# Optimization experiments

Hardware: AMD Instinct MI355X
Metric: run time of the kernel (lower is better)

## Reference

```python
import jax, jax.numpy as jnp
import numpy as np

B, T, S = 4, 128, 8192
HID, NH, NKV, HD = 2560, 8, 4, 256
INTER = 10240
WINDOW = 1024
SOFTCAP = 50.0
SCALING = 256 ** -0.5  # query_pre_attn_scalar ** -0.5
EPS = 1e-6
NEG = -2.3819763e38  # large negative for masking (matches Gemma mask value)
ROPE_THETA = 10000.0


def _rmsnorm(x, w):
    xf = x.astype(jnp.float32)
    o = xf * jax.lax.rsqrt(jnp.mean(xf * xf, axis=-1, keepdims=True) + EPS)
    return (o * (1.0 + w.astype(jnp.float32))).astype(x.dtype)


def _rope(x, cos, sin):
    # split-half rotation, matching torch apply_rotary_emb (chunk->complex->mul)
    d2 = x.shape[-1] // 2
    x1, x2 = x[..., :d2], x[..., d2:]
    c = cos[None, :, None, :]  # [1,T,1,D/2]
    s = sin[None, :, None, :]
    return jnp.concatenate([x1 * c - x2 * s, x1 * s + x2 * c], axis=-1)


def setup_inputs() -> dict:
    key = jax.random.key(0)
    ks = jax.random.split(key, 14)
    hidden_states = jax.random.normal(ks[0], (B, T, HID), jnp.float32)
    kv_write_indices = jnp.arange(T, dtype=jnp.int32)
    k_cache = jnp.zeros((B, S, NKV, HD), jnp.float32)
    v_cache = jnp.zeros((B, S, NKV, HD), jnp.float32)
    # rotary tables for positions 0..T-1
    inv = 1.0 / (ROPE_THETA ** (np.arange(0, HD, 2)[: HD // 2].astype(np.float32) / HD))
    fr = np.outer(np.arange(T, dtype=np.float32), inv).astype(np.float32)
    freqs_cos = jnp.asarray(np.cos(fr))
    freqs_sin = jnp.asarray(np.sin(fr))
    # masks: query i sits at absolute position i; cache slots >= T are unwritten
    qpos = jnp.arange(T)[:, None]
    kpos = jnp.arange(S)[None, :]
    causal = kpos <= qpos
    local = causal & ((qpos - kpos) < WINDOW)
    mask = jnp.broadcast_to(jnp.where(causal, 0.0, NEG)[None, None], (B, 1, T, S)).astype(jnp.float32)
    local_mask = jnp.broadcast_to(jnp.where(local, 0.0, NEG)[None, None], (B, 1, T, S)).astype(jnp.float32)
    sc = 0.02
    w_qkv = sc * jax.random.normal(ks[1], ((NH + 2 * NKV) * HD, HID), jnp.float32)
    w_o = sc * jax.random.normal(ks[2], (HID, NH * HD), jnp.float32)
    q_norm_w = 0.1 * jax.random.normal(ks[3], (HD,), jnp.float32)
    k_norm_w = 0.1 * jax.random.normal(ks[4], (HD,), jnp.float32)
    in_ln_w = 0.1 * jax.random.normal(ks[5], (HID,), jnp.float32)
    post_attn_ln_w = 0.1 * jax.random.normal(ks[6], (HID,), jnp.float32)
    pre_ffw_ln_w = 0.1 * jax.random.normal(ks[7], (HID,), jnp.float32)
    post_ffw_ln_w = 0.1 * jax.random.normal(ks[8], (HID,), jnp.float32)
    w_gate = sc * jax.random.normal(ks[9], (INTER, HID), jnp.float32)
    w_up = sc * jax.random.normal(ks[10], (INTER, HID), jnp.float32)
    w_down = sc * jax.random.normal(ks[11], (HID, INTER), jnp.float32)
    return {
        "hidden_states": hidden_states, "freqs_cos": freqs_cos, "freqs_sin": freqs_sin,
        "kv_write_indices": kv_write_indices, "k_cache": k_cache, "v_cache": v_cache,
        "mask": mask, "local_mask": local_mask,
        "w_qkv": w_qkv, "w_o": w_o, "q_norm_w": q_norm_w, "k_norm_w": k_norm_w,
        "in_ln_w": in_ln_w, "post_attn_ln_w": post_attn_ln_w,
        "pre_ffw_ln_w": pre_ffw_ln_w, "post_ffw_ln_w": post_ffw_ln_w,
        "w_gate": w_gate, "w_up": w_up, "w_down": w_down,
    }


def reference(hidden_states, freqs_cos, freqs_sin, kv_write_indices, k_cache, v_cache,
              mask, local_mask, w_qkv, w_o, q_norm_w, k_norm_w, in_ln_w,
              post_attn_ln_w, pre_ffw_ln_w, post_ffw_ln_w, w_gate, w_up, w_down):
    b, t, _ = hidden_states.shape
    residual = hidden_states
    h = _rmsnorm(hidden_states, in_ln_w)
    qkv = h @ w_qkv.T
    q_sz, kv_sz = NH * HD, NKV * HD
    xq = qkv[..., :q_sz].reshape(b, t, NH, HD)
    xk = qkv[..., q_sz:q_sz + kv_sz].reshape(b, t, NKV, HD)
    xv = qkv[..., q_sz + kv_sz:].reshape(b, t, NKV, HD)
    xq = _rmsnorm(xq, q_norm_w)  # QK-norm
    xk = _rmsnorm(xk, k_norm_w)
    xq = _rope(xq, freqs_cos, freqs_sin)
    xk = _rope(xk, freqs_cos, freqs_sin)
    kc = k_cache.at[:, kv_write_indices].set(xk)  # index_copy_ on dim 1
    vc = v_cache.at[:, kv_write_indices].set(xv)
    g = NH // NKV
    q = (xq * SCALING).reshape(b, t, NKV, g, HD)
    # GQA without repeat_interleave: group dim g shares each kv head
    scores = jnp.einsum('btkgd,bskd->bkgts', q, kc)
    scores = SOFTCAP * jnp.tanh(scores / SOFTCAP)  # logit softcapping
    scores = scores + local_mask[:, :, None]  # LOCAL_SLIDING -> use local mask
    probs = jax.nn.softmax(scores.astype(jnp.float32), axis=-1).astype(q.dtype)
    attn = jnp.einsum('bkgts,bskd->btkgd', probs, vc).reshape(b, t, NH * HD)
    attn = attn @ w_o.T
    h = residual + _rmsnorm(attn, post_attn_ln_w)
    residual = h
    x = _rmsnorm(h, pre_ffw_ln_w)
    gate = jax.nn.gelu(x @ w_gate.T, approximate=True)
    mlp = (gate * (x @ w_up.T)) @ w_down.T
    return residual + _rmsnorm(mlp, post_ffw_ln_w)
```

## Files before the change

kernel.cpp:

```cpp
#include <hip/hip_runtime.h>
#include <hip/hip_bf16.h>

#define B_ 4
#define T_ 128
#define HID 2560
#define NH 8
#define NKV 4
#define HD 256
#define INTER 10240
#define MROWS 512
#define EPS 1e-6f

typedef float f32x4 __attribute__((ext_vector_type(4)));
typedef __bf16 bf16x8 __attribute__((ext_vector_type(8)));

__device__ __forceinline__ unsigned short f2bf(float f){
  unsigned int u = __builtin_bit_cast(unsigned int, f);
  u += 0x7fffu + ((u >> 16) & 1u);
  return (unsigned short)(u >> 16);
}
__device__ __forceinline__ float bf2f(unsigned short u){
  unsigned int x = ((unsigned int)u) << 16;
  return __builtin_bit_cast(float, x);
}
__device__ __forceinline__ unsigned int cvtpk(float lo, float hi){
  unsigned int r;
  asm("v_cvt_pk_bf16_f32 %0, %1, %2" : "=v"(r) : "v"(lo), "v"(hi));
  return r;
}

__device__ __forceinline__ float bsum256(float v, float* buf){
  #pragma unroll
  for (int o = 32; o; o >>= 1) v += __shfl_xor(v, o);
  __syncthreads();
  if ((threadIdx.x & 63) == 0) buf[threadIdx.x >> 6] = v;
  __syncthreads();
  return buf[0] + buf[1] + buf[2] + buf[3];
}


__global__ __launch_bounds__(256) void rms_in(
    const float* __restrict__ x, const float* __restrict__ w,
    unsigned short* __restrict__ out)
{
  __shared__ float buf[4];
  const int r = blockIdx.x, tid = threadIdx.x;
  const float* xp = x + (size_t)r * HID;
  float v[10]; float ss = 0.f;
  #pragma unroll
  for (int j = 0; j < 10; j++){ v[j] = xp[tid + j*256]; ss += v[j]*v[j]; }
  ss = bsum256(ss, buf);
  float s = rsqrtf(ss * (1.f/HID) + EPS);
  #pragma unroll
  for (int j = 0; j < 10; j++){
    int i = tid + j*256;
    out[((size_t)(i >> 5) * MROWS + r) * 32 + (i & 31)] = f2bf(v[j] * s * (1.f + w[i]));
  }
}

__global__ __launch_bounds__(256, 2) void gemm_big(
    const unsigned short* __restrict__ Ap,
    const float* __restrict__ B0,
    const float* __restrict__ B1,
    int n_hi,
    unsigned short* __restrict__ C,
    int N, int K, int klen)
{
  __shared__ char Bs[2][128*64];
  const int tid = threadIdx.x;
  const int bid = (blockIdx.x & 7) * ((int)gridDim.x >> 3) + (blockIdx.x >> 3);
  const int bm = (bid & 1) << 8;
  const int bn = (bid >> 1) << 7;
  const int kt0 = (blockIdx.y * klen) >> 5;
  const int nt = klen >> 5;

  const int srow = tid >> 1, shalf = tid & 1;
  const float* Bb = (bn < n_hi) ? B0 : B1;
  const int bnr = (bn < n_hi) ? bn : (bn - n_hi);
  const float* BpG = Bb + (size_t)(bnr + srow) * K + (kt0 << 5) + (shalf << 4);

  const int wave = tid >> 6, lane = tid & 63;
  const int wm = (wave & 1) << 7;
  const int wn = (wave >> 1) << 6;
  const int fr = lane & 15, kq = lane >> 4;
  const int bslot = ((kq ^ ((fr >> 1) & 3)) << 4);
  const int brsw = (srow >> 1) & 3;
  const int s0 = (((2*shalf)     ^ brsw) << 4);
  const int s1 = (((2*shalf + 1) ^ brsw) << 4);

  const unsigned short* ApL = Ap + ((size_t)kt0 * MROWS + bm + wm + fr) * 32 + kq * 8;

  f32x4 acc[8][4];
  #pragma unroll
  for (int i = 0; i < 8; i++)
    #pragma unroll
    for (int j = 0; j < 4; j++)
      #pragma unroll
      for (int e = 0; e < 4; e++) acc[i][j][e] = 0.f;

  uint4 aR[8], aS[8];
  float4 rb0, rb1, rb2, rb3, sb0, sb1, sb2, sb3;

#define ISSUE_A(dst, tt) { const unsigned short* ap = ApL + (size_t)(tt) * 16384; \
  dst[0] = *(const uint4*)(ap);        dst[1] = *(const uint4*)(ap + 512); \
  dst[2] = *(const uint4*)(ap + 1024); dst[3] = *(const uint4*)(ap + 1536); \
  dst[4] = *(const uint4*)(ap + 2048); dst[5] = *(const uint4*)(ap + 2560); \
  dst[6] = *(const uint4*)(ap + 3072); dst[7] = *(const uint4*)(ap + 3584); }
#define LOAD_B(p0,p1,p2,p3, tt) { const float* bp = BpG + ((tt) << 5); \
  p0 = *(const float4*)(bp);     p1 = *(const float4*)(bp + 4); \
  p2 = *(const float4*)(bp + 8); p3 = *(const float4*)(bp + 12); }
#define WRITE_B(cur, b0,b1,b2,b3) { uint4 w0, w1; \
  w0.x = cvtpk(b0.x,b0.y); w0.y = cvtpk(b0.z,b0.w); \
  w0.z = cvtpk(b1.x,b1.y); w0.w = cvtpk(b1.z,b1.w); \
  w1.x = cvtpk(b2.x,b2.y); w1.y = cvtpk(b2.z,b2.w); \
  w1.z = cvtpk(b3.x,b3.y); w1.w = cvtpk(b3.z,b3.w); \
  char* bbase = &Bs[cur][srow*64]; \
  *(uint4*)(bbase + s0) = w0; \
  *(uint4*)(bbase + s1) = w1; }
#define BAR() { asm volatile("s_waitcnt lgkmcnt(0)" ::: "memory"); \
  __builtin_amdgcn_s_barrier(); }
#define COMPUTE(cur, aset) { const char* bb = Bs[cur]; \
  bf16x8 bfv[4]; \
  _Pragma("unroll") for (int ni = 0; ni < 4; ni++) \
    bfv[ni] = *(const bf16x8*)(bb + ((wn + ni*16 + fr) << 6) + bslot); \
  __builtin_amdgcn_s_setprio(1); \
  _Pragma("unroll") for (int mi = 0; mi < 8; mi++){ \
    bf16x8 af = __builtin_bit_cast(bf16x8, aset[mi]); \
    _Pragma("unroll") for (int ni = 0; ni < 4; ni++) \
      acc[mi][ni] = __builtin_amdgcn_mfma_f32_16x16x32_bf16(af, bfv[ni], acc[mi][ni], 0, 0, 0); } \
  __builtin_amdgcn_s_setprio(0); }

  ISSUE_A(aR, 0);
  LOAD_B(rb0,rb1,rb2,rb3, 0);
  LOAD_B(sb0,sb1,sb2,sb3, 1);

  for (int t = 0; t < nt; t += 2) {
    ISSUE_A(aS, t + 1);
    WRITE_B(0, rb0,rb1,rb2,rb3);
    BAR();
    if (t + 2 < nt) LOAD_B(rb0,rb1,rb2,rb3, t + 2);
    COMPUTE(0, aR);
    if (t + 2 < nt) ISSUE_A(aR, t + 2);
    WRITE_B(1, sb0,sb1,sb2,sb3);
    BAR();
    if (t + 3 < nt) LOAD_B(sb0,sb1,sb2,sb3, t + 3);
    COMPUTE(1, aS);
  }
#undef ISSUE_A
#undef LOAD_B
#undef WRITE_B
#undef BAR
#undef COMPUTE

  unsigned short* Cp = C + (size_t)blockIdx.y * MROWS * N;
  #pragma unroll
  for (int mi = 0; mi < 8; mi++) {
    #pragma unroll
    for (int ni = 0; ni < 4; ni++) {
      int m = bm + wm + mi*16 + kq*4;
      int n = bn + wn + ni*16 + fr;
      #pragma unroll
      for (int i = 0; i < 4; i++)
        Cp[(size_t)(m + i) * N + n] = f2bf(acc[mi][ni][i]);
    }
  }
}

__global__ __launch_bounds__(64) void qkv_post(
    const unsigned short* __restrict__ qkvp,
    const float* __restrict__ fcos, const float* __restrict__ fsin,
    const float* __restrict__ qnw, const float* __restrict__ knw,
    float* __restrict__ qout, float* __restrict__ kT, float* __restrict__ vout)
{
  const int row = blockIdx.x;
  const int hh  = blockIdx.y;
  const int b = row >> 7, t = row & 127;
  const int l = threadIdx.x;
  const size_t MS = (size_t)MROWS * 4096;
  const unsigned short* src = qkvp + (size_t)row * 4096 + hh * 256;
  float x[4];
  #pragma unroll
  for (int j = 0; j < 4; j++){
    int d = l + j*64;
    float v = 0.f;
    #pragma unroll
    for (int s = 0; s < 8; s++) v += bf2f(src[d + s*MS]);
    x[j] = v;
  }
  if (hh >= 12) {
    float* vp = vout + ((size_t)(b*NKV + (hh-12)) * T_ + t) * HD;
    #pragma unroll
    for (int j = 0; j < 4; j++) vp[l + j*64] = x[j];
    return;
  }
  float ss = x[0]*x[0] + x[1]*x[1] + x[2]*x[2] + x[3]*x[3];
  #pragma unroll
  for (int o = 32; o; o >>= 1) ss += __shfl_xor(ss, o);
  float r = rsqrtf(ss * (1.f/HD) + EPS);
  const float* nw = (hh < 8) ? qnw : knw;
  #pragma unroll
  for (int j = 0; j < 4; j++){ int d = l + j*64; x[j] = x[j] * r * (1.f + nw[d]); }
  float c0 = fcos[t*128 + l],      s0 = fsin[t*128 + l];
  float c1 = fcos[t*128 + l + 64], s1 = fsin[t*128 + l + 64];
  float y0 = x[0]*c0 - x[2]*s0;
  float y2 = x[0]*s0 + x[2]*c0;
  float y1 = x[1]*c1 - x[3]*s1;
  float y3 = x[1]*s1 + x[3]*c1;
  if (hh < 8) {
    float* qp = qout + ((size_t)(b*NH + hh) * T_ + t) * HD;
    const float sc = 0.0625f;
    qp[l] = y0*sc; qp[l+64] = y1*sc; qp[l+128] = y2*sc; qp[l+192] = y3*sc;
  } else {
    float* kp = kT + (size_t)(b*NKV + (hh-8)) * HD * T_;
    kp[(size_t)(l)*T_ + t] = y0;  kp[(size_t)(l+64)*T_ + t] = y1;
    kp[(size_t)(l+128)*T_ + t] = y2; kp[(size_t)(l+192)*T_ + t] = y3;
  }
}

__global__ __launch_bounds__(128) void attn_fwd(
    const float* __restrict__ q, const float* __restrict__ kT,
    const float* __restrict__ V, unsigned short* __restrict__ att)
{
  const int id = blockIdx.x;
  const int t = id & 127;
  const int h = (id >> 7) & 7;
  const int b = id >> 10;
  const int kvh = h >> 1;
  const int tid = threadIdx.x;
  __shared__ float qs[256];
  __shared__ float sc[128];
  __shared__ float red[128];
  const float* qp = q + (size_t)id * HD;
  qs[tid] = qp[tid]; qs[tid + 128] = qp[tid + 128];
  __syncthreads();
  const float* kp = kT + (size_t)(b*NKV + kvh) * HD * T_;
  float dot = 0.f;
  const bool valid = (tid <= t);
  if (valid) {
    #pragma unroll 8
    for (int d = 0; d < 256; d++) dot += qs[d] * kp[(size_t)d*T_ + tid];
  }
  float score = valid ? 50.f * tanhf(dot * 0.02f) : -3.0e38f;
  sc[tid] = score; red[tid] = score;
  __syncthreads();
  for (int o = 64; o; o >>= 1){ if (tid < o) red[tid] = fmaxf(red[tid], red[tid+o]); __syncthreads(); }
  float m = red[0];
  __syncthreads();
  float p = valid ? __expf(score - m) : 0.f;
  sc[tid] = p; red[tid] = p;
  __syncthreads();
  for (int o = 64; o; o >>= 1){ if (tid < o) red[tid] += red[tid+o]; __syncthreads(); }
  float inv = 1.f / red[0];
  const float* vp = V + (size_t)(b*NKV + kvh) * T_ * HD;
  float a0 = 0.f, a1 = 0.f;
  for (int s = 0; s <= t; s++){
    float ps = sc[s];
    a0 += ps * vp[(size_t)s*HD + tid];
    a1 += ps * vp[(size_t)s*HD + tid + 128];
  }
  const int row = b*T_ + t;
  const int c0 = h*256 + tid, c1 = c0 + 128;
  att[((size_t)(c0 >> 5) * MROWS + row) * 32 + (c0 & 31)] = f2bf(a0 * inv);
  att[((size_t)(c1 >> 5) * MROWS + row) * 32 + (c1 & 31)] = f2bf(a1 * inv);
}

__global__ __launch_bounds__(256) void post_attn_k(
    const unsigned short* __restrict__ op, const float* __restrict__ hs,
    const float* __restrict__ wpost, const float* __restrict__ wpre,
    float* __restrict__ h2, unsigned short* __restrict__ xout)
{
  __shared__ float buf[4];
  const int r = blockIdx.x, tid = threadIdx.x;
  const size_t MS = (size_t)MROWS * HID;
  float o[10]; float ss = 0.f;
  #pragma unroll
  for (int j = 0; j < 10; j++){
    size_t i = (size_t)r*HID + tid + j*256;
    float v = 0.f;
    #pragma unroll
    for (int s = 0; s < 16; s++) v += bf2f(op[i + s*MS]);
    o[j] = v; ss += v*v;
  }
  ss = bsum256(ss, buf);
  float s = rsqrtf(ss*(1.f/HID) + EPS);
  float h[10]; float s2 = 0.f;
  #pragma unroll
  for (int j = 0; j < 10; j++){
    int i = tid + j*256;
    float hv = hs[(size_t)r*HID + i] + o[j]*s*(1.f + wpost[i]);
    h[j] = hv; h2[(size_t)r*HID + i] = hv; s2 += hv*hv;
  }
  s2 = bsum256(s2, buf);
  float sc2 = rsqrtf(s2*(1.f/HID) + EPS);
  #pragma unroll
  for (int j = 0; j < 10; j++){
    int i = tid + j*256;
    xout[((size_t)(i >> 5) * MROWS + r) * 32 + (i & 31)] = f2bf(h[j]*sc2*(1.f + wpre[i]));
  }
}

__global__ __launch_bounds__(256) void act_fuse(
    const unsigned short* __restrict__ gu,
    unsigned short* __restrict__ act)
{
  const int r = blockIdx.x;
  const size_t MS = (size_t)MROWS * 20480;
  const unsigned short* rowp = gu + (size_t)r * 20480;
  for (int c = threadIdx.x; c < INTER; c += 256){
    float g = 0.f, u = 0.f;
    #pragma unroll
    for (int s = 0; s < 4; s++){
      g += bf2f(rowp[s*MS + c]);
      u += bf2f(rowp[s*MS + c + INTER]);
    }
    float tt = tanhf(0.7978845608f * (g + 0.044715f * g*g*g));
    float ge = 0.5f * g * (1.f + tt);
    act[((size_t)(c >> 5) * MROWS + r) * 32 + (c & 31)] = f2bf(ge * u);
  }
}

__global__ __launch_bounds__(256) void final_k(
    const unsigned short* __restrict__ dp, const float* __restrict__ h2,
    const float* __restrict__ w, float* __restrict__ out)
{
  __shared__ float buf[4];
  const int r = blockIdx.x, tid = threadIdx.x;
  const size_t MS = (size_t)MROWS * HID;
  float m[10]; float ss = 0.f;
  #pragma unroll
  for (int j = 0; j < 10; j++){
    size_t i = (size_t)r*HID + tid + j*256;
    float v = 0.f;
    #pragma unroll
    for (int s = 0; s < 16; s++) v += bf2f(dp[i + s*MS]);
    m[j] = v; ss += v*v;
  }
  ss = bsum256(ss, buf);
  float s = rsqrtf(ss*(1.f/HID) + EPS);
  #pragma unroll
  for (int j = 0; j < 10; j++){
    int i = tid + j*256;
    out[(size_t)r*HID + i] = h2[(size_t)r*HID + i] + m[j]*s*(1.f + w[i]);
  }
}

extern "C" void kernel_launch(void* const* d_in, const int* in_sizes, int n_in,
                              void* d_out, int out_size, void* d_ws, size_t ws_size,
                              hipStream_t stream)
{
  const float* hs     = (const float*)d_in[0];
  const float* fcos   = (const float*)d_in[1];
  const float* fsin   = (const float*)d_in[2];
  const float* w_qkv  = (const float*)d_in[8];
  const float* w_o    = (const float*)d_in[9];
  const float* qnw    = (const float*)d_in[10];
  const float* knw    = (const float*)d_in[11];
  const float* in_ln  = (const float*)d_in[12];
  const float* w_post = (const float*)d_in[13];
  const float* w_pre  = (const float*)d_in[14];
  const float* w_pffw = (const float*)d_in[15];
  const float* w_gate = (const float*)d_in[16];
  const float* w_up   = (const float*)d_in[17];
  const float* w_down = (const float*)d_in[18];
  float* out = (float*)d_out;

  char* p = (char*)d_ws;
  auto alloc = [&](size_t bytes)->void*{ void* r = p; p += (bytes + 255) & ~(size_t)255; return r; };
  void* P0 = alloc((size_t)4*MROWS*20480*2);
  void* P1 = alloc((size_t)16*MROWS*HID*2);
  unsigned short* h_b   = (unsigned short*)alloc((size_t)MROWS*HID*2);
  float* qbuf           = (float*)alloc((size_t)B_*NH*T_*HD*4);
  float* kT             = (float*)alloc((size_t)B_*NKV*HD*T_*4);
  float* vbuf           = (float*)alloc((size_t)B_*NKV*T_*HD*4);
  unsigned short* att_b = (unsigned short*)alloc((size_t)MROWS*2048*2);
  float* h2             = (float*)alloc((size_t)MROWS*HID*4);
  unsigned short* x_b   = (unsigned short*)alloc((size_t)MROWS*HID*2);
  unsigned short* act_b = (unsigned short*)alloc((size_t)MROWS*INTER*2);

  unsigned short* qkv_p = (unsigned short*)P0;
  unsigned short* gu_p  = (unsigned short*)P0;
  unsigned short* o_p   = (unsigned short*)P1;
  unsigned short* down_p= (unsigned short*)P1;

  rms_in<<<MROWS, 256, 0, stream>>>(hs, in_ln, h_b);
  gemm_big<<<dim3(64, 8), 256, 0, stream>>>(h_b, w_qkv, w_qkv, 1<<30, qkv_p, 4096, 2560, 320);
  qkv_post<<<dim3(MROWS, 16), 64, 0, stream>>>(qkv_p, fcos, fsin, qnw, knw, qbuf, kT, vbuf);
  attn_fwd<<<B_*NH*T_, 128, 0, stream>>>(qbuf, kT, vbuf, att_b);
  gemm_big<<<dim3(40, 16), 256, 0, stream>>>(att_b, w_o, w_o, 1<<30, o_p, 2560, 2048, 128);
  post_attn_k<<<MROWS, 256, 0, stream>>>(o_p, hs, w_post, w_pre, h2, x_b);
  gemm_big<<<dim3(320, 4), 256, 0, stream>>>(x_b, w_gate, w_up, 10240, gu_p, 20480, 2560, 640);
  act_fuse<<<MROWS, 256, 0, stream>>>(gu_p, act_b);
  gemm_big<<<dim3(40, 16), 256, 0, stream>>>(act_b, w_down, w_down, 1<<30, down_p, 2560, 10240, 640);
  final_k<<<MROWS, 256, 0, stream>>>(down_p, h2, w_pffw, out);
}
```

Measured before the change: 353.8 us.

## Stream fp32 weights into LDS via direct global-to-LDS loads with 4-stage ring

The GEMM's weight-tile staging changes from register loads plus convert-and-store to global_load_lds async copies of raw fp32 into a 4-slot XOR-swizzled LDS ring. Conversion to bf16 now happens at LDS read time, and barriers are gated on vmcnt. The intent is to remove register pressure and staging instructions and to deepen prefetch. In exchange LDS use grows to 64KB and the per-compute conversion work rises. The down-projection split-K also goes from 16 to 32, and act_fuse gets a 2D grid for more parallelism, which adds partial-sum traffic in final_k.

After: 378.0 us. 6.9% more time.

```diff
diff --git a/kernel.cpp b/kernel.cpp
--- a/kernel.cpp
+++ b/kernel.cpp
@@ -28,6 +28,11 @@
   asm("v_cvt_pk_bf16_f32 %0, %1, %2" : "=v"(r) : "v"(lo), "v"(hi));
   return r;
 }
+__device__ __forceinline__ void glds16(const void* g, void* l){
+  __builtin_amdgcn_global_load_lds(
+      (const __attribute__((address_space(1))) void*)g,
+      (__attribute__((address_space(3))) void*)l, 16, 0, 0);
+}
 
 __device__ __forceinline__ float bsum256(float v, float* buf){
   #pragma unroll
@@ -66,7 +71,7 @@
     unsigned short* __restrict__ C,
     int N, int K, int klen)
 {
-  __shared__ char Bs[2][128*64];
+  __shared__ char Bs4[4 * 16384];
   const int tid = threadIdx.x;
   const int bid = (blockIdx.x & 7) * ((int)gridDim.x >> 3) + (blockIdx.x >> 3);
   const int bm = (bid & 1) << 8;
@@ -74,19 +79,16 @@
   const int kt0 = (blockIdx.y * klen) >> 5;
   const int nt = klen >> 5;
 
-  const int srow = tid >> 1, shalf = tid & 1;
+  const int w = tid >> 6, l = tid & 63;
   const float* Bb = (bn < n_hi) ? B0 : B1;
   const int bnr = (bn < n_hi) ? bn : (bn - n_hi);
-  const float* BpG = Bb + (size_t)(bnr + srow) * K + (kt0 << 5) + (shalf << 4);
-
-  const int wave = tid >> 6, lane = tid & 63;
-  const int wm = (wave & 1) << 7;
-  const int wn = (wave >> 1) << 6;
-  const int fr = lane & 15, kq = lane >> 4;
-  const int bslot = ((kq ^ ((fr >> 1) & 3)) << 4);
-  const int brsw = (srow >> 1) & 3;
-  const int s0 = (((2*shalf)     ^ brsw) << 4);
-  const int s1 = (((2*shalf + 1) ^ brsw) << 4);
+
+  const int grow_l = l >> 3;
+  const int gchunk = l & 7;
+
+  const int wm = (w & 1) << 7;
+  const int wn = (w >> 1) << 6;
+  const int fr = l & 15, kq = l >> 4;
 
   const unsigned short* ApL = Ap + ((size_t)kt0 * MROWS + bm + wm + fr) * 32 + kq * 8;
 
@@ -99,58 +101,68 @@
       for (int e = 0; e < 4; e++) acc[i][j][e] = 0.f;
 
   uint4 aR[8], aS[8];
-  float4 rb0, rb1, rb2, rb3, sb0, sb1, sb2, sb3;
 
 #define ISSUE_A(dst, tt) { const unsigned short* ap = ApL + (size_t)(tt) * 16384; \
   dst[0] = *(const uint4*)(ap);        dst[1] = *(const uint4*)(ap + 512); \
   dst[2] = *(const uint4*)(ap + 1024); dst[3] = *(const uint4*)(ap + 1536); \
   dst[4] = *(const uint4*)(ap + 2048); dst[5] = *(const uint4*)(ap + 2560); \
   dst[6] = *(const uint4*)(ap + 3072); dst[7] = *(const uint4*)(ap + 3584); }
-#define LOAD_B(p0,p1,p2,p3, tt) { const float* bp = BpG + ((tt) << 5); \
-  p0 = *(const float4*)(bp);     p1 = *(const float4*)(bp + 4); \
-  p2 = *(const float4*)(bp + 8); p3 = *(const float4*)(bp + 12); }
-#define WRITE_B(cur, b0,b1,b2,b3) { uint4 w0, w1; \
-  w0.x = cvtpk(b0.x,b0.y); w0.y = cvtpk(b0.z,b0.w); \
-  w0.z = cvtpk(b1.x,b1.y); w0.w = cvtpk(b1.z,b1.w); \
-  w1.x = cvtpk(b2.x,b2.y); w1.y = cvtpk(b2.z,b2.w); \
-  w1.z = cvtpk(b3.x,b3.y); w1.w = cvtpk(b3.z,b3.w); \
-  char* bbase = &Bs[cur][srow*64]; \
-  *(uint4*)(bbase + s0) = w0; \
-  *(uint4*)(bbase + s1) = w1; }
-#define BAR() { asm volatile("s_waitcnt lgkmcnt(0)" ::: "memory"); \
-  __builtin_amdgcn_s_barrier(); }
-#define COMPUTE(cur, aset) { const char* bb = Bs[cur]; \
+#define GLDS_B(tt, slot) { const int ktf = (kt0 + (tt)) << 5; \
+  char* dstb = Bs4 + ((slot) << 14) + (w << 12); \
+  _Pragma("unroll") for (int g = 0; g < 4; g++){ \
+    int row = (w << 5) + (g << 3) + grow_l; \
+    const float* src = Bb + (size_t)(bnr + row) * K + ktf + ((gchunk ^ (row & 7)) << 2); \
+    glds16(src, dstb + (g << 10)); } }
+#define VM(n) asm volatile("s_waitcnt vmcnt(" #n ")" ::: "memory")
+#define COMPUTE(slot, aset) { const char* bb = Bs4 + ((slot) << 14); \
   bf16x8 bfv[4]; \
-  _Pragma("unroll") for (int ni = 0; ni < 4; ni++) \
-    bfv[ni] = *(const bf16x8*)(bb + ((wn + ni*16 + fr) << 6) + bslot); \
+  _Pragma("unroll") for (int ni = 0; ni < 4; ni++){ \
+    int row = wn + ni*16 + fr; \
+    const char* rbase = bb + (row << 7); \
+    int sw = row & 7; \
+    f32x4 lo = *(const f32x4*)(rbase + ((( 2*kq   ) ^ sw) << 4)); \
+    f32x4 hi = *(const f32x4*)(rbase + ((( 2*kq+1 ) ^ sw) << 4)); \
+    union { unsigned int u[4]; bf16x8 v; } pk; \
+    pk.u[0] = cvtpk(lo[0], lo[1]); pk.u[1] = cvtpk(lo[2], lo[3]); \
+    pk.u[2] = cvtpk(hi[0], hi[1]); pk.u[3] = cvtpk(hi[2], hi[3]); \
+    bfv[ni] = pk.v; } \
   __builtin_amdgcn_s_setprio(1); \
   _Pragma("unroll") for (int mi = 0; mi < 8; mi++){ \
     bf16x8 af = __builtin_bit_cast(bf16x8, aset[mi]); \
     _Pragma("unroll") for (int ni = 0; ni < 4; ni++) \
       acc[mi][ni] = __builtin_amdgcn_mfma_f32_16x16x32_bf16(af, bfv[ni], acc[mi][ni], 0, 0, 0); } \
   __builtin_amdgcn_s_setprio(0); }
+#define MIN_(a,b) ((a)<(b)?(a):(b))
 
   ISSUE_A(aR, 0);
-  LOAD_B(rb0,rb1,rb2,rb3, 0);
-  LOAD_B(sb0,sb1,sb2,sb3, 1);
-
-  for (int t = 0; t < nt; t += 2) {
-    ISSUE_A(aS, t + 1);
-    WRITE_B(0, rb0,rb1,rb2,rb3);
-    BAR();
-    if (t + 2 < nt) LOAD_B(rb0,rb1,rb2,rb3, t + 2);
-    COMPUTE(0, aR);
-    if (t + 2 < nt) ISSUE_A(aR, t + 2);
-    WRITE_B(1, sb0,sb1,sb2,sb3);
-    BAR();
-    if (t + 3 < nt) LOAD_B(sb0,sb1,sb2,sb3, t + 3);
-    COMPUTE(1, aS);
+  GLDS_B(0, 0); GLDS_B(1, 1); GLDS_B(2, 2);
+  ISSUE_A(aS, MIN_(1, nt-1));
+  VM(16);
+  __builtin_amdgcn_s_barrier();
+  GLDS_B(MIN_(3, nt-1), 3);
+  COMPUTE(0, aR);
+  ISSUE_A(aR, MIN_(2, nt-1));
+  VM(24);
+  __builtin_amdgcn_s_barrier();
+  GLDS_B(MIN_(4, nt-1), 0);
+  COMPUTE(1, aS);
+  for (int t = 2; t < nt; t += 2) {
+    ISSUE_A(aS, MIN_(t+1, nt-1));
+    VM(32);
+    __builtin_amdgcn_s_barrier();
+    GLDS_B(MIN_(t+3, nt-1), (t+3) & 3);
+    COMPUTE(t & 3, aR);
+    ISSUE_A(aR, MIN_(t+2, nt-1));
+    VM(32);
+    __builtin_amdgcn_s_barrier();
+    GLDS_B(MIN_(t+4, nt-1), t & 3);
+    COMPUTE((t+1) & 3, aS);
   }
 #undef ISSUE_A
-#undef LOAD_B
-#undef WRITE_B
-#undef BAR
+#undef GLDS_B
+#undef VM
 #undef COMPUTE
+#undef MIN_
 
   unsigned short* Cp = C + (size_t)blockIdx.y * MROWS * N;
   #pragma unroll
@@ -304,9 +316,10 @@
     unsigned short* __restrict__ act)
 {
   const int r = blockIdx.x;
+  const int c0 = blockIdx.y * 2560;
   const size_t MS = (size_t)MROWS * 20480;
   const unsigned short* rowp = gu + (size_t)r * 20480;
-  for (int c = threadIdx.x; c < INTER; c += 256){
+  for (int c = c0 + threadIdx.x; c < c0 + 2560; c += 256){
     float g = 0.f, u = 0.f;
     #pragma unroll
     for (int s = 0; s < 4; s++){
@@ -332,7 +345,7 @@
     size_t i = (size_t)r*HID + tid + j*256;
     float v = 0.f;
     #pragma unroll
-    for (int s = 0; s < 16; s++) v += bf2f(dp[i + s*MS]);
+    for (int s = 0; s < 32; s++) v += bf2f(dp[i + s*MS]);
     m[j] = v; ss += v*v;
   }
   ss = bsum256(ss, buf);
@@ -367,7 +380,7 @@
   char* p = (char*)d_ws;
   auto alloc = [&](size_t bytes)->void*{ void* r = p; p += (bytes + 255) & ~(size_t)255; return r; };
   void* P0 = alloc((size_t)4*MROWS*20480*2);
-  void* P1 = alloc((size_t)16*MROWS*HID*2);
+  void* P1 = alloc((size_t)32*MROWS*HID*2);
   unsigned short* h_b   = (unsigned short*)alloc((size_t)MROWS*HID*2);
   float* qbuf           = (float*)alloc((size_t)B_*NH*T_*HD*4);
   float* kT             = (float*)alloc((size_t)B_*NKV*HD*T_*4);
@@ -389,7 +402,7 @@
   gemm_big<<<dim3(40, 16), 256, 0, stream>>>(att_b, w_o, w_o, 1<<30, o_p, 2560, 2048, 128);
   post_attn_k<<<MROWS, 256, 0, stream>>>(o_p, hs, w_post, w_pre, h2, x_b);
   gemm_big<<<dim3(320, 4), 256, 0, stream>>>(x_b, w_gate, w_up, 10240, gu_p, 20480, 2560, 640);
-  act_fuse<<<MROWS, 256, 0, stream>>>(gu_p, act_b);
-  gemm_big<<<dim3(40, 16), 256, 0, stream>>>(act_b, w_down, w_down, 1<<30, down_p, 2560, 10240, 640);
+  act_fuse<<<dim3(MROWS, 4), 256, 0, stream>>>(gu_p, act_b);
+  gemm_big<<<dim3(40, 32), 256, 0, stream>>>(act_b, w_down, w_down, 1<<30, down_p, 2560, 10240, 320);
   final_k<<<MROWS, 256, 0, stream>>>(down_p, h2, w_pffw, out);
 }
```
